# Kernel tuning notes

Hardware: AMD Instinct MI355X
Metric: run time of the kernel (lower is better)

## Reference

```python
import jax, jax.numpy as jnp
import numpy as np

B, N, M, C, KV, H = 2, 1024, 2048, 1024, 768, 16
D = C // H
SCALE = D ** -0.5  # qk_scale defaults to head_dim**-0.5


def setup_inputs() -> dict:
    key = jax.random.key(0)
    ks = jax.random.split(key, 8)
    return {
        "q": jax.random.normal(ks[0], (B, N, C), jnp.float32),
        "kv": jax.random.normal(ks[1], (B, M, KV), jnp.float32),
        "alibi_bias": jax.random.normal(ks[2], (B, H, N, M), jnp.float32) * 0.02,
        "padding_mask": jax.random.randint(ks[3], (B, M), 0, 2).astype(bool),
        "Wq": jax.random.normal(ks[4], (C, C), jnp.float32) * 0.02,
        "Wkv": jax.random.normal(ks[5], (2 * C, KV), jnp.float32) * 0.02,
        "Wproj": jax.random.normal(ks[6], (C, C), jnp.float32) * 0.02,
        "bproj": jnp.zeros((C,), jnp.float32),
    }


def reference(q, kv, alibi_bias, Wq, Wkv, Wproj, bproj, padding_mask):
    Bq, Nq, Cq = q.shape
    # q projection -> (B, H, N, D)
    qh = (q @ Wq.T).reshape(Bq, Nq, H, D).transpose(0, 2, 1, 3)
    # kv projection -> (2, B, H, M, D)
    kvp = (kv @ Wkv.T).reshape(Bq, -1, 2, H, D).transpose(2, 0, 3, 1, 4)
    k, v = kvp[0], kvp[1]
    # scaled dot-product scores (B, H, N, M)
    attn = jnp.einsum('bhnd,bhmd->bhnm', qh * SCALE, k)
    attn = attn + alibi_bias
    attn = jnp.where(padding_mask[:, None, None, :], -jnp.inf, attn)
    # softmax in fp32, cast back to q dtype (matches torch softmax(dtype=float32))
    attn = jax.nn.softmax(attn.astype(jnp.float32), axis=-1).astype(q.dtype)
    x = jnp.einsum('bhnm,bhmd->bhnd', attn, v).transpose(0, 2, 1, 3).reshape(Bq, Nq, Cq)
    return x @ Wproj.T + bproj
```

## Files before the change

### kernel.cpp

```cpp
#include <hip/hip_runtime.h>
#include <hip/hip_bf16.h>
#include <hip/hip_fp16.h>

#define B_  2
#define N_  1024
#define M_  2048
#define C_  1024
#define KV_ 768
#define H_  16
#define D_  64

typedef _Float16 half8 __attribute__((ext_vector_type(8)));
typedef float f32x4 __attribute__((ext_vector_type(4)));

__device__ inline void gload16(const _Float16* g, _Float16* l) {
    __builtin_amdgcn_global_load_lds(
        (const __attribute__((address_space(1))) unsigned int*)g,
        (__attribute__((address_space(3))) unsigned int*)l, 16, 0, 0);
}

#define NQ4  (B_ * N_ * C_ / 4)
#define NKV4 (B_ * M_ * KV_ / 4)
#define NWQ4 (C_ * C_ / 4)
#define NWK4 (2 * C_ * KV_ / 4)
#define NTOT4 (NQ4 + NKV4 + NWQ4 + NWK4 + NWQ4)

__global__ __launch_bounds__(256)
void cvt_all(const float* __restrict__ q, const float* __restrict__ kv,
             const float* __restrict__ Wq, const float* __restrict__ Wkv,
             const float* __restrict__ Wp,
             _Float16* __restrict__ qh, _Float16* __restrict__ kvh,
             _Float16* __restrict__ Wqh, _Float16* __restrict__ Wkvh,
             _Float16* __restrict__ Wph)
{
    int i = blockIdx.x * 256 + threadIdx.x;
    if (i >= NTOT4) return;
    const float* s; _Float16* d; int off; float sc = 1.0f;
    if (i < NQ4)                          { s = q;   d = qh;   off = i; sc = 0.125f; }
    else if (i < NQ4 + NKV4)              { s = kv;  d = kvh;  off = i - NQ4; }
    else if (i < NQ4 + NKV4 + NWQ4)       { s = Wq;  d = Wqh;  off = i - NQ4 - NKV4; }
    else if (i < NQ4 + NKV4 + NWQ4 + NWK4){ s = Wkv; d = Wkvh; off = i - NQ4 - NKV4 - NWQ4; }
    else                                  { s = Wp;  d = Wph;  off = i - NQ4 - NKV4 - NWQ4 - NWK4; }
    float4 v = ((const float4*)s)[off];
    union { _Float16 h[4]; unsigned long long u; } pk;
    pk.h[0] = (_Float16)(v.x * sc); pk.h[1] = (_Float16)(v.y * sc);
    pk.h[2] = (_Float16)(v.z * sc); pk.h[3] = (_Float16)(v.w * sc);
    ((unsigned long long*)d)[off] = pk.u;
}

template<int ND, int KD, int EPI>
__device__ __forceinline__
void gemm_body(const _Float16* A, const _Float16* Bm, void* out0, void* out1,
               _Float16* As, _Float16* Bs, int bx, int by)
{
    const int tid  = threadIdx.x;
    const int lane = tid & 63;
    const int w    = tid >> 6;
    const int l16  = lane & 15;
    const int quad = lane >> 4;
    const int wm   = w >> 1, wn = w & 1;
    const int m0   = by * 128;
    const int n0   = bx * 128;

    const int srow = tid >> 2;
    const int scol = ((tid & 3) ^ (srow & 3)) * 8;
    const int ldso = srow * 32 + (tid & 3) * 8;

    f32x4 acc[4][4];
    {
        f32x4 z = {0.f, 0.f, 0.f, 0.f};
        for (int i = 0; i < 4; i++) for (int j = 0; j < 4; j++) acc[i][j] = z;
    }

    for (int k0 = 0; k0 < KD; k0 += 32) {
        __syncthreads();
        gload16(A  + (size_t)(m0 + srow)      * KD + k0 + scol, As + ldso);
        gload16(A  + (size_t)(m0 + 64 + srow) * KD + k0 + scol, As + 64 * 32 + ldso);
        gload16(Bm + (size_t)(n0 + srow)      * KD + k0 + scol, Bs + ldso);
        gload16(Bm + (size_t)(n0 + 64 + srow) * KD + k0 + scol, Bs + 64 * 32 + ldso);
        __syncthreads();

        half8 af[4], bf[4];
        #pragma unroll
        for (int i = 0; i < 4; i++) {
            int r = wm * 64 + i * 16 + l16;
            af[i] = *(const half8*)&As[r * 32 + ((quad ^ (r & 3)) * 8)];
        }
        #pragma unroll
        for (int j = 0; j < 4; j++) {
            int r = wn * 64 + j * 16 + l16;
            bf[j] = *(const half8*)&Bs[r * 32 + ((quad ^ (r & 3)) * 8)];
        }
        #pragma unroll
        for (int i = 0; i < 4; i++)
            #pragma unroll
            for (int j = 0; j < 4; j++)
                acc[i][j] = __builtin_amdgcn_mfma_f32_16x16x32_f16(af[i], bf[j], acc[i][j], 0, 0, 0);
    }

    #pragma unroll
    for (int i = 0; i < 4; i++)
        #pragma unroll
        for (int j = 0; j < 4; j++) {
            int mb = m0 + wm * 64 + i * 16 + quad * 4;
            int n  = n0 + wn * 64 + j * 16 + l16;
            if (EPI == 0) {
                #pragma unroll
                for (int r = 0; r < 4; r++)
                    ((_Float16*)out0)[(size_t)(mb + r) * ND + n] = (_Float16)acc[i][j][r];
            } else {
                int b = mb >> 11, ml = mb & 2047;
                if (n < C_) {
                    int h = n >> 6, d = n & 63;
                    #pragma unroll
                    for (int r = 0; r < 4; r++)
                        ((_Float16*)out0)[((size_t)(b * H_ + h) * M_ + ml + r) * D_ + d] =
                            (_Float16)acc[i][j][r];
                } else {
                    int h = (n >> 6) & 15, d = n & 63;
                    union { _Float16 h4[4]; unsigned long long u; } pk;
                    #pragma unroll
                    for (int r = 0; r < 4; r++) pk.h4[r] = (_Float16)acc[i][j][r];
                    *(unsigned long long*)&((_Float16*)out1)[((size_t)(b * H_ + h) * D_ + d) * M_ + ml] = pk.u;
                }
            }
        }
}

__global__ __launch_bounds__(256)
void qkv_gemm(const _Float16* __restrict__ qh, const _Float16* __restrict__ Wqh,
              _Float16* __restrict__ qp,
              const _Float16* __restrict__ kvh, const _Float16* __restrict__ Wkvh,
              _Float16* __restrict__ k_ws, _Float16* __restrict__ v_ws)
{
    __shared__ _Float16 As[128 * 32];
    __shared__ _Float16 Bs[128 * 32];
    int id = blockIdx.x;
    if (id < 128)
        gemm_body<C_, C_, 0>(qh, Wqh, qp, nullptr, As, Bs, id & 7, id >> 3);
    else {
        int r = id - 128;
        gemm_body<2 * C_, KV_, 1>(kvh, Wkvh, k_ws, v_ws, As, Bs, r & 15, r >> 4);
    }
}

__global__ __launch_bounds__(256)
void outproj(const _Float16* __restrict__ A, const _Float16* __restrict__ Bm,
             float* __restrict__ out, const float* __restrict__ bias)
{
    __shared__ _Float16 As[64 * 32];
    __shared__ _Float16 Bs[64 * 32];

    const int tid  = threadIdx.x;
    const int lane = tid & 63;
    const int w    = tid >> 6;
    const int l16  = lane & 15;
    const int quad = lane >> 4;
    const int wm   = w >> 1, wn = w & 1;
    const int m0   = blockIdx.y * 64;
    const int n0   = blockIdx.x * 64;

    const int srow = tid >> 2;
    const int scol = ((tid & 3) ^ (srow & 3)) * 8;
    const int ldso = srow * 32 + (tid & 3) * 8;

    f32x4 acc[2][2];
    {
        f32x4 z = {0.f, 0.f, 0.f, 0.f};
        for (int i = 0; i < 2; i++) for (int j = 0; j < 2; j++) acc[i][j] = z;
    }

    for (int k0 = 0; k0 < C_; k0 += 32) {
        __syncthreads();
        gload16(A  + (size_t)(m0 + srow) * C_ + k0 + scol, As + ldso);
        gload16(Bm + (size_t)(n0 + srow) * C_ + k0 + scol, Bs + ldso);
        __syncthreads();

        half8 af[2], bf[2];
        #pragma unroll
        for (int i = 0; i < 2; i++) {
            int r = wm * 32 + i * 16 + l16;
            af[i] = *(const half8*)&As[r * 32 + ((quad ^ (r & 3)) * 8)];
        }
        #pragma unroll
        for (int j = 0; j < 2; j++) {
            int r = wn * 32 + j * 16 + l16;
            bf[j] = *(const half8*)&Bs[r * 32 + ((quad ^ (r & 3)) * 8)];
        }
        #pragma unroll
        for (int i = 0; i < 2; i++)
            #pragma unroll
            for (int j = 0; j < 2; j++)
                acc[i][j] = __builtin_amdgcn_mfma_f32_16x16x32_f16(af[i], bf[j], acc[i][j], 0, 0, 0);
    }

    #pragma unroll
    for (int i = 0; i < 2; i++)
        #pragma unroll
        for (int j = 0; j < 2; j++)
            #pragma unroll
            for (int r = 0; r < 4; r++) {
                int m = m0 + wm * 32 + i * 16 + quad * 4 + r;
                int n = n0 + wn * 32 + j * 16 + l16;
                out[(size_t)m * C_ + n] = acc[i][j][r] + bias[n];
            }
}

__global__ __launch_bounds__(256)
void flash_attn(const _Float16* __restrict__ qw, const _Float16* __restrict__ kw,
                const _Float16* __restrict__ vw, const float* __restrict__ alibi,
                const void* __restrict__ pmask, _Float16* __restrict__ xw)
{
    __shared__ _Float16 Ks[128 * 64];
    __shared__ _Float16 Vs[64 * 128];
    __shared__ _Float16 Ps[4][16][136];
    __shared__ int mflag;

    const int tid  = threadIdx.x;
    const int lane = tid & 63;
    const int w    = tid >> 6;
    const int l16  = lane & 15;
    const int quad = lane >> 4;
    const int bh   = blockIdx.y;
    const int b    = bh >> 4;
    const int h    = bh & 15;
    const int n0   = blockIdx.x * 64;

    if (tid < 64) {
        unsigned a = ((const unsigned*)pmask)[tid] & 0xFFFFFF00u;
        unsigned long long anyset = __ballot(a != 0);
        if (tid == 0) mflag = (anyset == 0ull) ? 1 : 0;
    }
    __syncthreads();
    const int mi = mflag;

    half8 qf[2];
    {
        const _Float16* qp = qw + ((size_t)(b * N_ + n0 + w * 16 + l16) * C_) + h * 64 + quad * 8;
        qf[0] = *(const half8*)qp;
        qf[1] = *(const half8*)(qp + 32);
    }

    f32x4 accO[4];
    float rs[4];
    {
        f32x4 z = {0.f, 0.f, 0.f, 0.f};
        for (int i = 0; i < 4; i++) accO[i] = z;
    }
    #pragma unroll
    for (int r = 0; r < 4; r++) rs[r] = 0.f;

    const _Float16* kbase = kw + (size_t)bh * (M_ * D_);
    const _Float16* vbase = vw + (size_t)bh * (D_ * M_);
    const float*    abase = alibi + (size_t)bh * ((size_t)N_ * M_) + (size_t)n0 * M_
                          + (size_t)(w * 16 + quad * 4) * M_;
    const unsigned char* pm8  = (const unsigned char*)pmask;
    const int*           pm32 = (const int*)pmask;

    for (int m0 = 0; m0 < M_; m0 += 128) {
        __syncthreads();
        #pragma unroll
        for (int i = 0; i < 4; i++) {
            int idx = tid + 256 * i;
            int kr = idx >> 3, kp = idx & 7;
            gload16(kbase + (size_t)(m0 + kr) * D_ + ((kp ^ (kr & 7)) * 8), Ks + idx * 8);
            int vr = idx >> 4, vp = idx & 15;
            gload16(vbase + (size_t)vr * M_ + m0 + ((vp ^ (vr & 15)) * 8), Vs + idx * 8);
        }
        __syncthreads();

        float al[8][4];
        int   mk[8];
        #pragma unroll
        for (int j = 0; j < 8; j++) {
            int mcol = m0 + j * 16 + l16;
            mk[j] = mi ? pm32[b * M_ + mcol] : (int)pm8[b * M_ + mcol];
            const float* ap = abase + mcol;
            #pragma unroll
            for (int r = 0; r < 4; r++) al[j][r] = ap[(size_t)r * M_];
        }

        f32x4 s[8];
        {
            f32x4 z = {0.f, 0.f, 0.f, 0.f};
            for (int j = 0; j < 8; j++) s[j] = z;
        }
        #pragma unroll
        for (int j = 0; j < 8; j++) {
            int row = j * 16 + l16;
            half8 kf0 = *(const half8*)&Ks[row * 64 + ((quad ^ (row & 7)) * 8)];
            half8 kf1 = *(const half8*)&Ks[row * 64 + (((4 + quad) ^ (row & 7)) * 8)];
            s[j] = __builtin_amdgcn_mfma_f32_16x16x32_f16(qf[0], kf0, s[j], 0, 0, 0);
            s[j] = __builtin_amdgcn_mfma_f32_16x16x32_f16(qf[1], kf1, s[j], 0, 0, 0);
        }

        #pragma unroll
        for (int j = 0; j < 8; j++)
            #pragma unroll
            for (int r = 0; r < 4; r++) {
                float sv = fminf(s[j][r] + al[j][r], 11.0f);
                float p  = exp2f(sv * 1.44269504f);
                p = mk[j] ? 0.f : p;
                rs[r] += p;
                Ps[w][quad * 4 + r][j * 16 + l16] = (_Float16)p;
            }

        #pragma unroll
        for (int kk = 0; kk < 4; kk++) {
            half8 pf = *(const half8*)&Ps[w][l16][kk * 32 + quad * 8];
            #pragma unroll
            for (int dt = 0; dt < 4; dt++) {
                int vrow = dt * 16 + l16;
                half8 vf = *(const half8*)&Vs[vrow * 128 + (((kk * 4 + quad) ^ (vrow & 15)) * 8)];
                accO[dt] = __builtin_amdgcn_mfma_f32_16x16x32_f16(pf, vf, accO[dt], 0, 0, 0);
            }
        }
    }

    #pragma unroll
    for (int off = 1; off < 16; off <<= 1)
        #pragma unroll
        for (int r = 0; r < 4; r++) rs[r] += __shfl_xor(rs[r], off, 64);
    float inv[4];
    #pragma unroll
    for (int r = 0; r < 4; r++) inv[r] = 1.0f / rs[r];

    #pragma unroll
    for (int dt = 0; dt < 4; dt++)
        #pragma unroll
        for (int r = 0; r < 4; r++) {
            int n = n0 + w * 16 + quad * 4 + r;
            xw[(size_t)(b * N_ + n) * C_ + h * 64 + dt * 16 + l16] =
                (_Float16)(accO[dt][r] * inv[r]);
        }
}

extern "C" void kernel_launch(void* const* d_in, const int* in_sizes, int n_in,
                              void* d_out, int out_size, void* d_ws, size_t ws_size,
                              hipStream_t stream)
{
    const float* q     = (const float*)d_in[0];
    const float* kv    = (const float*)d_in[1];
    const float* alibi = (const float*)d_in[2];
    const void*  pmask = d_in[3];
    const float* Wq    = (const float*)d_in[4];
    const float* Wkv   = (const float*)d_in[5];
    const float* Wproj = (const float*)d_in[6];
    const float* bproj = (const float*)d_in[7];
    float* out = (float*)d_out;

    const size_t MB = 1u << 20;
    char* ws = (char*)d_ws;
    _Float16* qh     = (_Float16*)(ws + 0 * MB);
    _Float16* kvh    = (_Float16*)(ws + 4 * MB);
    _Float16* Wqh    = (_Float16*)(ws + 12 * MB);
    _Float16* Wkvh   = (_Float16*)(ws + 14 * MB);
    _Float16* Wprojh = (_Float16*)(ws + 18 * MB);
    _Float16* qp     = (_Float16*)(ws + 20 * MB);
    _Float16* k_ws   = (_Float16*)(ws + 24 * MB);
    _Float16* v_ws   = (_Float16*)(ws + 33 * MB);
    _Float16* x_ws   = (_Float16*)(ws + 42 * MB);

    cvt_all<<<(NTOT4 + 255) / 256, 256, 0, stream>>>(
        q, kv, Wq, Wkv, Wproj, qh, kvh, Wqh, Wkvh, Wprojh);

    qkv_gemm<<<640, 256, 0, stream>>>(qh, Wqh, qp, kvh, Wkvh, k_ws, v_ws);

    flash_attn<<<dim3(N_ / 64, B_ * H_), 256, 0, stream>>>(
        qp, k_ws, v_ws, alibi, pmask, x_ws);

    outproj<<<dim3(C_ / 64, (B_ * N_) / 64), 256, 0, stream>>>(
        x_ws, Wprojh, out, bproj);
}
```

Before: 461.6 us.

## Fuse all stages into one persistent kernel with software grid barriers

Replaces the four separate launches (convert, QKV GEMM, flash attention, output projection) with a single persistent kernel of 512 blocks that runs each stage in turn, separated by atomic-counter grid barriers. The QKV GEMM tiles are spread over the fixed grid, with the first 128 blocks taking a second tile. The aim is to remove inter-kernel launch gaps and drain/fill bubbles. In exchange it relies on all 512 blocks being co-resident (launch bounds of 2 blocks per CU), adds a zeroing launch and spin-wait barriers with a timeout break, and may limit registers for the attention stage.

```diff
diff --git a/kernel.cpp b/kernel.cpp
--- a/kernel.cpp
+++ b/kernel.cpp
@@ -10,6 +10,8 @@
 #define H_  16
 #define D_  64
 
+#define NBLK 512
+
 typedef _Float16 half8 __attribute__((ext_vector_type(8)));
 typedef float f32x4 __attribute__((ext_vector_type(4)));
 
@@ -25,27 +27,25 @@
 #define NWK4 (2 * C_ * KV_ / 4)
 #define NTOT4 (NQ4 + NKV4 + NWQ4 + NWK4 + NWQ4)
 
-__global__ __launch_bounds__(256)
-void cvt_all(const float* __restrict__ q, const float* __restrict__ kv,
-             const float* __restrict__ Wq, const float* __restrict__ Wkv,
-             const float* __restrict__ Wp,
-             _Float16* __restrict__ qh, _Float16* __restrict__ kvh,
-             _Float16* __restrict__ Wqh, _Float16* __restrict__ Wkvh,
-             _Float16* __restrict__ Wph)
-{
-    int i = blockIdx.x * 256 + threadIdx.x;
-    if (i >= NTOT4) return;
-    const float* s; _Float16* d; int off; float sc = 1.0f;
-    if (i < NQ4)                          { s = q;   d = qh;   off = i; sc = 0.125f; }
-    else if (i < NQ4 + NKV4)              { s = kv;  d = kvh;  off = i - NQ4; }
-    else if (i < NQ4 + NKV4 + NWQ4)       { s = Wq;  d = Wqh;  off = i - NQ4 - NKV4; }
-    else if (i < NQ4 + NKV4 + NWQ4 + NWK4){ s = Wkv; d = Wkvh; off = i - NQ4 - NKV4 - NWQ4; }
-    else                                  { s = Wp;  d = Wph;  off = i - NQ4 - NKV4 - NWQ4 - NWK4; }
-    float4 v = ((const float4*)s)[off];
-    union { _Float16 h[4]; unsigned long long u; } pk;
-    pk.h[0] = (_Float16)(v.x * sc); pk.h[1] = (_Float16)(v.y * sc);
-    pk.h[2] = (_Float16)(v.z * sc); pk.h[3] = (_Float16)(v.w * sc);
-    ((unsigned long long*)d)[off] = pk.u;
+__device__ __forceinline__ void grid_barrier(unsigned int* bar, unsigned int target)
+{
+    __syncthreads();
+    if (threadIdx.x == 0) {
+        __threadfence();
+        __hip_atomic_fetch_add(bar, 1u, __ATOMIC_RELEASE, __HIP_MEMORY_SCOPE_AGENT);
+        int spins = 0;
+        while (__hip_atomic_load(bar, __ATOMIC_ACQUIRE, __HIP_MEMORY_SCOPE_AGENT) < target) {
+            __builtin_amdgcn_s_sleep(16);
+            if (++spins > 100000) break;
+        }
+    }
+    __syncthreads();
+    __threadfence();
+}
+
+__global__ void zero_bar(unsigned int* bar)
+{
+    if (threadIdx.x == 0) *bar = 0;
 }
 
 template<int ND, int KD, int EPI>
@@ -127,212 +127,240 @@
         }
 }
 
-__global__ __launch_bounds__(256)
-void qkv_gemm(const _Float16* __restrict__ qh, const _Float16* __restrict__ Wqh,
-              _Float16* __restrict__ qp,
-              const _Float16* __restrict__ kvh, const _Float16* __restrict__ Wkvh,
-              _Float16* __restrict__ k_ws, _Float16* __restrict__ v_ws)
-{
-    __shared__ _Float16 As[128 * 32];
-    __shared__ _Float16 Bs[128 * 32];
-    int id = blockIdx.x;
-    if (id < 128)
-        gemm_body<C_, C_, 0>(qh, Wqh, qp, nullptr, As, Bs, id & 7, id >> 3);
-    else {
-        int r = id - 128;
-        gemm_body<2 * C_, KV_, 1>(kvh, Wkvh, k_ws, v_ws, As, Bs, r & 15, r >> 4);
-    }
-}
-
-__global__ __launch_bounds__(256)
-void outproj(const _Float16* __restrict__ A, const _Float16* __restrict__ Bm,
-             float* __restrict__ out, const float* __restrict__ bias)
-{
-    __shared__ _Float16 As[64 * 32];
-    __shared__ _Float16 Bs[64 * 32];
-
-    const int tid  = threadIdx.x;
-    const int lane = tid & 63;
-    const int w    = tid >> 6;
-    const int l16  = lane & 15;
-    const int quad = lane >> 4;
-    const int wm   = w >> 1, wn = w & 1;
-    const int m0   = blockIdx.y * 64;
-    const int n0   = blockIdx.x * 64;
-
-    const int srow = tid >> 2;
-    const int scol = ((tid & 3) ^ (srow & 3)) * 8;
-    const int ldso = srow * 32 + (tid & 3) * 8;
-
-    f32x4 acc[2][2];
+#define SMEM_BYTES 50192
+
+__global__ __launch_bounds__(256, 2)
+void fused(const float* __restrict__ q, const float* __restrict__ kv,
+           const float* __restrict__ alibi, const void* __restrict__ pmask,
+           const float* __restrict__ Wq, const float* __restrict__ Wkv,
+           const float* __restrict__ Wp, const float* __restrict__ bias,
+           float* __restrict__ out,
+           _Float16* __restrict__ qh, _Float16* __restrict__ kvh,
+           _Float16* __restrict__ Wqh, _Float16* __restrict__ Wkvh,
+           _Float16* __restrict__ Wph,
+           _Float16* __restrict__ qp, _Float16* __restrict__ k_ws,
+           _Float16* __restrict__ v_ws, _Float16* __restrict__ x_ws,
+           unsigned int* __restrict__ bar)
+{
+    __shared__ __align__(16) unsigned char smem[SMEM_BYTES];
+    const int tid = threadIdx.x;
+    const int bid = blockIdx.x;
+
+    for (int i = bid * 256 + tid; i < NTOT4; i += NBLK * 256) {
+        const float* s; _Float16* d; int off; float sc = 1.0f;
+        if (i < NQ4)                          { s = q;   d = qh;   off = i; sc = 0.125f; }
+        else if (i < NQ4 + NKV4)              { s = kv;  d = kvh;  off = i - NQ4; }
+        else if (i < NQ4 + NKV4 + NWQ4)       { s = Wq;  d = Wqh;  off = i - NQ4 - NKV4; }
+        else if (i < NQ4 + NKV4 + NWQ4 + NWK4){ s = Wkv; d = Wkvh; off = i - NQ4 - NKV4 - NWQ4; }
+        else                                  { s = Wp;  d = Wph;  off = i - NQ4 - NKV4 - NWQ4 - NWK4; }
+        float4 v = ((const float4*)s)[off];
+        union { _Float16 h[4]; unsigned long long u; } pk;
+        pk.h[0] = (_Float16)(v.x * sc); pk.h[1] = (_Float16)(v.y * sc);
+        pk.h[2] = (_Float16)(v.z * sc); pk.h[3] = (_Float16)(v.w * sc);
+        ((unsigned long long*)d)[off] = pk.u;
+    }
+    grid_barrier(bar, NBLK);
+
     {
-        f32x4 z = {0.f, 0.f, 0.f, 0.f};
-        for (int i = 0; i < 2; i++) for (int j = 0; j < 2; j++) acc[i][j] = z;
-    }
-
-    for (int k0 = 0; k0 < C_; k0 += 32) {
+        _Float16* As = (_Float16*)smem;
+        _Float16* Bs = (_Float16*)(smem + 128 * 32 * 2);
+        int t = (bid < 384) ? (128 + bid) : (bid - 384);
+        for (;;) {
+            if (t < 128)
+                gemm_body<C_, C_, 0>(qh, Wqh, qp, nullptr, As, Bs, t & 7, t >> 3);
+            else {
+                int r = t - 128;
+                gemm_body<2 * C_, KV_, 1>(kvh, Wkvh, k_ws, v_ws, As, Bs, r & 15, r >> 4);
+            }
+            if (bid < 128 && t < 512) { t = 512 + bid; continue; }
+            break;
+        }
+    }
+    grid_barrier(bar, 2 * NBLK);
+
+    {
+        _Float16* Ks = (_Float16*)(smem);
+        _Float16* Vs = (_Float16*)(smem + 16384);
+        _Float16* Ps = (_Float16*)(smem + 32768);
+        int* mflagp  = (int*)(smem + 50176);
+
+        const int lane = tid & 63;
+        const int w    = tid >> 6;
+        const int l16  = lane & 15;
+        const int quad = lane >> 4;
+        const int wk = (bid & 7) * 64 + (bid >> 3);
+        const int bh = wk >> 4;
+        const int b  = bh >> 4;
+        const int h  = bh & 15;
+        const int n0 = (wk & 15) * 64;
+
+        if (tid < 64) {
+            unsigned a = ((const unsigned*)pmask)[tid] & 0xFFFFFF00u;
+            unsigned long long anyset = __ballot(a != 0);
+            if (tid == 0) *mflagp = (anyset == 0ull) ? 1 : 0;
+        }
         __syncthreads();
-        gload16(A  + (size_t)(m0 + srow) * C_ + k0 + scol, As + ldso);
-        gload16(Bm + (size_t)(n0 + srow) * C_ + k0 + scol, Bs + ldso);
-        __syncthreads();
-
-        half8 af[2], bf[2];
-        #pragma unroll
-        for (int i = 0; i < 2; i++) {
-            int r = wm * 32 + i * 16 + l16;
-            af[i] = *(const half8*)&As[r * 32 + ((quad ^ (r & 3)) * 8)];
-        }
-        #pragma unroll
-        for (int j = 0; j < 2; j++) {
-            int r = wn * 32 + j * 16 + l16;
-            bf[j] = *(const half8*)&Bs[r * 32 + ((quad ^ (r & 3)) * 8)];
-        }
-        #pragma unroll
-        for (int i = 0; i < 2; i++)
-            #pragma unroll
-            for (int j = 0; j < 2; j++)
-                acc[i][j] = __builtin_amdgcn_mfma_f32_16x16x32_f16(af[i], bf[j], acc[i][j], 0, 0, 0);
-    }
-
-    #pragma unroll
-    for (int i = 0; i < 2; i++)
-        #pragma unroll
-        for (int j = 0; j < 2; j++)
-            #pragma unroll
-            for (int r = 0; r < 4; r++) {
-                int m = m0 + wm * 32 + i * 16 + quad * 4 + r;
-                int n = n0 + wn * 32 + j * 16 + l16;
-                out[(size_t)m * C_ + n] = acc[i][j][r] + bias[n];
-            }
-}
-
-__global__ __launch_bounds__(256)
-void flash_attn(const _Float16* __restrict__ qw, const _Float16* __restrict__ kw,
-                const _Float16* __restrict__ vw, const float* __restrict__ alibi,
-                const void* __restrict__ pmask, _Float16* __restrict__ xw)
-{
-    __shared__ _Float16 Ks[128 * 64];
-    __shared__ _Float16 Vs[64 * 128];
-    __shared__ _Float16 Ps[4][16][136];
-    __shared__ int mflag;
-
-    const int tid  = threadIdx.x;
-    const int lane = tid & 63;
-    const int w    = tid >> 6;
-    const int l16  = lane & 15;
-    const int quad = lane >> 4;
-    const int bh   = blockIdx.y;
-    const int b    = bh >> 4;
-    const int h    = bh & 15;
-    const int n0   = blockIdx.x * 64;
-
-    if (tid < 64) {
-        unsigned a = ((const unsigned*)pmask)[tid] & 0xFFFFFF00u;
-        unsigned long long anyset = __ballot(a != 0);
-        if (tid == 0) mflag = (anyset == 0ull) ? 1 : 0;
-    }
-    __syncthreads();
-    const int mi = mflag;
-
-    half8 qf[2];
-    {
-        const _Float16* qp = qw + ((size_t)(b * N_ + n0 + w * 16 + l16) * C_) + h * 64 + quad * 8;
-        qf[0] = *(const half8*)qp;
-        qf[1] = *(const half8*)(qp + 32);
-    }
-
-    f32x4 accO[4];
-    float rs[4];
-    {
-        f32x4 z = {0.f, 0.f, 0.f, 0.f};
-        for (int i = 0; i < 4; i++) accO[i] = z;
-    }
-    #pragma unroll
-    for (int r = 0; r < 4; r++) rs[r] = 0.f;
-
-    const _Float16* kbase = kw + (size_t)bh * (M_ * D_);
-    const _Float16* vbase = vw + (size_t)bh * (D_ * M_);
-    const float*    abase = alibi + (size_t)bh * ((size_t)N_ * M_) + (size_t)n0 * M_
-                          + (size_t)(w * 16 + quad * 4) * M_;
-    const unsigned char* pm8  = (const unsigned char*)pmask;
-    const int*           pm32 = (const int*)pmask;
-
-    for (int m0 = 0; m0 < M_; m0 += 128) {
-        __syncthreads();
-        #pragma unroll
-        for (int i = 0; i < 4; i++) {
-            int idx = tid + 256 * i;
-            int kr = idx >> 3, kp = idx & 7;
-            gload16(kbase + (size_t)(m0 + kr) * D_ + ((kp ^ (kr & 7)) * 8), Ks + idx * 8);
-            int vr = idx >> 4, vp = idx & 15;
-            gload16(vbase + (size_t)vr * M_ + m0 + ((vp ^ (vr & 15)) * 8), Vs + idx * 8);
-        }
-        __syncthreads();
-
-        float al[8][4];
-        int   mk[8];
-        #pragma unroll
-        for (int j = 0; j < 8; j++) {
-            int mcol = m0 + j * 16 + l16;
-            mk[j] = mi ? pm32[b * M_ + mcol] : (int)pm8[b * M_ + mcol];
-            const float* ap = abase + mcol;
-            #pragma unroll
-            for (int r = 0; r < 4; r++) al[j][r] = ap[(size_t)r * M_];
-        }
-
-        f32x4 s[8];
+        const int mi = *mflagp;
+
+        half8 qf[2];
+        {
+            const _Float16* qptr = qp + ((size_t)(b * N_ + n0 + w * 16 + l16) * C_) + h * 64 + quad * 8;
+            qf[0] = *(const half8*)qptr;
+            qf[1] = *(const half8*)(qptr + 32);
+        }
+
+        f32x4 accO[4];
+        float rs[4];
         {
             f32x4 z = {0.f, 0.f, 0.f, 0.f};
-            for (int j = 0; j < 8; j++) s[j] = z;
-        }
-        #pragma unroll
-        for (int j = 0; j < 8; j++) {
-            int row = j * 16 + l16;
-            half8 kf0 = *(const half8*)&Ks[row * 64 + ((quad ^ (row & 7)) * 8)];
-            half8 kf1 = *(const half8*)&Ks[row * 64 + (((4 + quad) ^ (row & 7)) * 8)];
-            s[j] = __builtin_amdgcn_mfma_f32_16x16x32_f16(qf[0], kf0, s[j], 0, 0, 0);
-            s[j] = __builtin_amdgcn_mfma_f32_16x16x32_f16(qf[1], kf1, s[j], 0, 0, 0);
-        }
-
-        #pragma unroll
-        for (int j = 0; j < 8; j++)
+            for (int i = 0; i < 4; i++) accO[i] = z;
+        }
+        #pragma unroll
+        for (int r = 0; r < 4; r++) rs[r] = 0.f;
+
+        const _Float16* kbase = k_ws + (size_t)bh * (M_ * D_);
+        const _Float16* vbase = v_ws + (size_t)bh * (D_ * M_);
+        const float*    abase = alibi + (size_t)bh * ((size_t)N_ * M_) + (size_t)n0 * M_
+                              + (size_t)(w * 16 + quad * 4) * M_;
+        const unsigned char* pm8  = (const unsigned char*)pmask;
+        const int*           pm32 = (const int*)pmask;
+
+        for (int m0 = 0; m0 < M_; m0 += 128) {
+            __syncthreads();
+            #pragma unroll
+            for (int i = 0; i < 4; i++) {
+                int idx = tid + 256 * i;
+                int kr = idx >> 3, kp = idx & 7;
+                gload16(kbase + (size_t)(m0 + kr) * D_ + ((kp ^ (kr & 7)) * 8), Ks + idx * 8);
+                int vr = idx >> 4, vp = idx & 15;
+                gload16(vbase + (size_t)vr * M_ + m0 + ((vp ^ (vr & 15)) * 8), Vs + idx * 8);
+            }
+            __syncthreads();
+
+            float al[8][4];
+            int   mk[8];
+            #pragma unroll
+            for (int j = 0; j < 8; j++) {
+                int mcol = m0 + j * 16 + l16;
+                mk[j] = mi ? pm32[b * M_ + mcol] : (int)pm8[b * M_ + mcol];
+                const float* ap = abase + mcol;
+                #pragma unroll
+                for (int r = 0; r < 4; r++) al[j][r] = ap[(size_t)r * M_];
+            }
+
+            f32x4 s[8];
+            {
+                f32x4 z = {0.f, 0.f, 0.f, 0.f};
+                for (int j = 0; j < 8; j++) s[j] = z;
+            }
+            #pragma unroll
+            for (int j = 0; j < 8; j++) {
+                int row = j * 16 + l16;
+                half8 kf0 = *(const half8*)&Ks[row * 64 + ((quad ^ (row & 7)) * 8)];
+                half8 kf1 = *(const half8*)&Ks[row * 64 + (((4 + quad) ^ (row & 7)) * 8)];
+                s[j] = __builtin_amdgcn_mfma_f32_16x16x32_f16(qf[0], kf0, s[j], 0, 0, 0);
+                s[j] = __builtin_amdgcn_mfma_f32_16x16x32_f16(qf[1], kf1, s[j], 0, 0, 0);
+            }
+
+            #pragma unroll
+            for (int j = 0; j < 8; j++)
+                #pragma unroll
+                for (int r = 0; r < 4; r++) {
+                    float sv = fminf(s[j][r] + al[j][r], 11.0f);
+                    float p  = exp2f(sv * 1.44269504f);
+                    p = mk[j] ? 0.f : p;
+                    rs[r] += p;
+                    Ps[(w * 16 + quad * 4 + r) * 136 + j * 16 + l16] = (_Float16)p;
+                }
+
+            #pragma unroll
+            for (int kk = 0; kk < 4; kk++) {
+                half8 pf = *(const half8*)&Ps[(w * 16 + l16) * 136 + kk * 32 + quad * 8];
+                #pragma unroll
+                for (int dt = 0; dt < 4; dt++) {
+                    int vrow = dt * 16 + l16;
+                    half8 vf = *(const half8*)&Vs[vrow * 128 + (((kk * 4 + quad) ^ (vrow & 15)) * 8)];
+                    accO[dt] = __builtin_amdgcn_mfma_f32_16x16x32_f16(pf, vf, accO[dt], 0, 0, 0);
+                }
+            }
+        }
+
+        #pragma unroll
+        for (int off = 1; off < 16; off <<= 1)
+            #pragma unroll
+            for (int r = 0; r < 4; r++) rs[r] += __shfl_xor(rs[r], off, 64);
+        float inv[4];
+        #pragma unroll
+        for (int r = 0; r < 4; r++) inv[r] = 1.0f / rs[r];
+
+        #pragma unroll
+        for (int dt = 0; dt < 4; dt++)
             #pragma unroll
             for (int r = 0; r < 4; r++) {
-                float sv = fminf(s[j][r] + al[j][r], 11.0f);
-                float p  = exp2f(sv * 1.44269504f);
-                p = mk[j] ? 0.f : p;
-                rs[r] += p;
-                Ps[w][quad * 4 + r][j * 16 + l16] = (_Float16)p;
-            }
-
-        #pragma unroll
-        for (int kk = 0; kk < 4; kk++) {
-            half8 pf = *(const half8*)&Ps[w][l16][kk * 32 + quad * 8];
-            #pragma unroll
-            for (int dt = 0; dt < 4; dt++) {
-                int vrow = dt * 16 + l16;
-                half8 vf = *(const half8*)&Vs[vrow * 128 + (((kk * 4 + quad) ^ (vrow & 15)) * 8)];
-                accO[dt] = __builtin_amdgcn_mfma_f32_16x16x32_f16(pf, vf, accO[dt], 0, 0, 0);
-            }
-        }
-    }
-
-    #pragma unroll
-    for (int off = 1; off < 16; off <<= 1)
-        #pragma unroll
-        for (int r = 0; r < 4; r++) rs[r] += __shfl_xor(rs[r], off, 64);
-    float inv[4];
-    #pragma unroll
-    for (int r = 0; r < 4; r++) inv[r] = 1.0f / rs[r];
-
-    #pragma unroll
-    for (int dt = 0; dt < 4; dt++)
-        #pragma unroll
-        for (int r = 0; r < 4; r++) {
-            int n = n0 + w * 16 + quad * 4 + r;
-            xw[(size_t)(b * N_ + n) * C_ + h * 64 + dt * 16 + l16] =
-                (_Float16)(accO[dt][r] * inv[r]);
-        }
+                int n = n0 + w * 16 + quad * 4 + r;
+                x_ws[(size_t)(b * N_ + n) * C_ + h * 64 + dt * 16 + l16] =
+                    (_Float16)(accO[dt][r] * inv[r]);
+            }
+    }
+    grid_barrier(bar, 3 * NBLK);
+
+    {
+        _Float16* As = (_Float16*)smem;
+        _Float16* Bs = (_Float16*)(smem + 64 * 32 * 2);
+
+        const int lane = tid & 63;
+        const int w    = tid >> 6;
+        const int l16  = lane & 15;
+        const int quad = lane >> 4;
+        const int wm   = w >> 1, wn = w & 1;
+        const int m0   = (bid >> 4) * 64;
+        const int n0   = (bid & 15) * 64;
+
+        const int srow = tid >> 2;
+        const int scol = ((tid & 3) ^ (srow & 3)) * 8;
+        const int ldso = srow * 32 + (tid & 3) * 8;
+
+        f32x4 acc[2][2];
+        {
+            f32x4 z = {0.f, 0.f, 0.f, 0.f};
+            for (int i = 0; i < 2; i++) for (int j = 0; j < 2; j++) acc[i][j] = z;
+        }
+
+        for (int k0 = 0; k0 < C_; k0 += 32) {
+            __syncthreads();
+            gload16(x_ws + (size_t)(m0 + srow) * C_ + k0 + scol, As + ldso);
+            gload16(Wph  + (size_t)(n0 + srow) * C_ + k0 + scol, Bs + ldso);
+            __syncthreads();
+
+            half8 af[2], bf[2];
+            #pragma unroll
+            for (int i = 0; i < 2; i++) {
+                int r = wm * 32 + i * 16 + l16;
+                af[i] = *(const half8*)&As[r * 32 + ((quad ^ (r & 3)) * 8)];
+            }
+            #pragma unroll
+            for (int j = 0; j < 2; j++) {
+                int r = wn * 32 + j * 16 + l16;
+                bf[j] = *(const half8*)&Bs[r * 32 + ((quad ^ (r & 3)) * 8)];
+            }
+            #pragma unroll
+            for (int i = 0; i < 2; i++)
+                #pragma unroll
+                for (int j = 0; j < 2; j++)
+                    acc[i][j] = __builtin_amdgcn_mfma_f32_16x16x32_f16(af[i], bf[j], acc[i][j], 0, 0, 0);
+        }
+
+        #pragma unroll
+        for (int i = 0; i < 2; i++)
+            #pragma unroll
+            for (int j = 0; j < 2; j++)
+                #pragma unroll
+                for (int r = 0; r < 4; r++) {
+                    int m = m0 + wm * 32 + i * 16 + quad * 4 + r;
+                    int n = n0 + wn * 32 + j * 16 + l16;
+                    out[(size_t)m * C_ + n] = acc[i][j][r] + bias[n];
+                }
+    }
 }
 
 extern "C" void kernel_launch(void* const* d_in, const int* in_sizes, int n_in,
@@ -360,15 +388,10 @@
     _Float16* k_ws   = (_Float16*)(ws + 24 * MB);
     _Float16* v_ws   = (_Float16*)(ws + 33 * MB);
     _Float16* x_ws   = (_Float16*)(ws + 42 * MB);
-
-    cvt_all<<<(NTOT4 + 255) / 256, 256, 0, stream>>>(
-        q, kv, Wq, Wkv, Wproj, qh, kvh, Wqh, Wkvh, Wprojh);
-
-    qkv_gemm<<<640, 256, 0, stream>>>(qh, Wqh, qp, kvh, Wkvh, k_ws, v_ws);
-
-    flash_attn<<<dim3(N_ / 64, B_ * H_), 256, 0, stream>>>(
-        qp, k_ws, v_ws, alibi, pmask, x_ws);
-
-    outproj<<<dim3(C_ / 64, (B_ * N_) / 64), 256, 0, stream>>>(
-        x_ws, Wprojh, out, bproj);
-}
+    unsigned int* bar = (unsigned int*)(ws + 63 * MB);
+
+    zero_bar<<<1, 64, 0, stream>>>(bar);
+    fused<<<NBLK, 256, 0, stream>>>(
+        q, kv, alibi, pmask, Wq, Wkv, Wproj, bproj, out,
+        qh, kvh, Wqh, Wkvh, Wprojh, qp, k_ws, v_ws, x_ws, bar);
+}
```

Result: slower. 824.5 us (+78.6%).

## Read K/V directly from global in attention, remap blocks across XCDs, stream alibi nontemporally

Applied to the files above, without the earlier changes.

The attention kernel no longer stages K and V tiles in shared memory with barriers. Each wave now loads its MFMA operands straight from global memory and relies on L2 for reuse. The grid becomes 1D with a block-index swizzle so that blocks sharing a (batch, head) land on the same XCD's L2, and the alibi bias is read with nontemporal loads to avoid polluting the cache. This removes the LDS traffic and both per-iteration __syncthreads. In exchange, each of the four waves refetches the same K/V data from cache, and the global loads are less coalesced.

```diff
diff --git a/kernel.cpp b/kernel.cpp
--- a/kernel.cpp
+++ b/kernel.cpp
@@ -211,28 +211,23 @@
                 const _Float16* __restrict__ vw, const float* __restrict__ alibi,
                 const void* __restrict__ pmask, _Float16* __restrict__ xw)
 {
-    __shared__ _Float16 Ks[128 * 64];
-    __shared__ _Float16 Vs[64 * 128];
     __shared__ _Float16 Ps[4][16][136];
-    __shared__ int mflag;
 
     const int tid  = threadIdx.x;
     const int lane = tid & 63;
     const int w    = tid >> 6;
     const int l16  = lane & 15;
     const int quad = lane >> 4;
-    const int bh   = blockIdx.y;
-    const int b    = bh >> 4;
-    const int h    = bh & 15;
-    const int n0   = blockIdx.x * 64;
-
-    if (tid < 64) {
-        unsigned a = ((const unsigned*)pmask)[tid] & 0xFFFFFF00u;
-        unsigned long long anyset = __ballot(a != 0);
-        if (tid == 0) mflag = (anyset == 0ull) ? 1 : 0;
-    }
-    __syncthreads();
-    const int mi = mflag;
+
+    const int bid = blockIdx.x;
+    const int wk  = (bid & 7) * 64 + (bid >> 3);
+    const int bh  = wk >> 4;
+    const int b   = bh >> 4;
+    const int h   = bh & 15;
+    const int n0  = (wk & 15) * 64;
+
+    unsigned am = ((const unsigned*)pmask)[lane] & 0xFFFFFF00u;
+    const int mi = (__ballot(am != 0) == 0ull) ? 1 : 0;
 
     half8 qf[2];
     {
@@ -258,17 +253,6 @@
     const int*           pm32 = (const int*)pmask;
 
     for (int m0 = 0; m0 < M_; m0 += 128) {
-        __syncthreads();
-        #pragma unroll
-        for (int i = 0; i < 4; i++) {
-            int idx = tid + 256 * i;
-            int kr = idx >> 3, kp = idx & 7;
-            gload16(kbase + (size_t)(m0 + kr) * D_ + ((kp ^ (kr & 7)) * 8), Ks + idx * 8);
-            int vr = idx >> 4, vp = idx & 15;
-            gload16(vbase + (size_t)vr * M_ + m0 + ((vp ^ (vr & 15)) * 8), Vs + idx * 8);
-        }
-        __syncthreads();
-
         float al[8][4];
         int   mk[8];
         #pragma unroll
@@ -277,7 +261,8 @@
             mk[j] = mi ? pm32[b * M_ + mcol] : (int)pm8[b * M_ + mcol];
             const float* ap = abase + mcol;
             #pragma unroll
-            for (int r = 0; r < 4; r++) al[j][r] = ap[(size_t)r * M_];
+            for (int r = 0; r < 4; r++)
+                al[j][r] = __builtin_nontemporal_load(ap + (size_t)r * M_);
         }
 
         f32x4 s[8];
@@ -288,8 +273,9 @@
         #pragma unroll
         for (int j = 0; j < 8; j++) {
             int row = j * 16 + l16;
-            half8 kf0 = *(const half8*)&Ks[row * 64 + ((quad ^ (row & 7)) * 8)];
-            half8 kf1 = *(const half8*)&Ks[row * 64 + (((4 + quad) ^ (row & 7)) * 8)];
+            const _Float16* kp = kbase + (size_t)(m0 + row) * D_ + quad * 8;
+            half8 kf0 = *(const half8*)kp;
+            half8 kf1 = *(const half8*)(kp + 32);
             s[j] = __builtin_amdgcn_mfma_f32_16x16x32_f16(qf[0], kf0, s[j], 0, 0, 0);
             s[j] = __builtin_amdgcn_mfma_f32_16x16x32_f16(qf[1], kf1, s[j], 0, 0, 0);
         }
@@ -310,8 +296,8 @@
             half8 pf = *(const half8*)&Ps[w][l16][kk * 32 + quad * 8];
             #pragma unroll
             for (int dt = 0; dt < 4; dt++) {
-                int vrow = dt * 16 + l16;
-                half8 vf = *(const half8*)&Vs[vrow * 128 + (((kk * 4 + quad) ^ (vrow & 15)) * 8)];
+                const _Float16* vp = vbase + (size_t)(dt * 16 + l16) * M_ + m0 + kk * 32 + quad * 8;
+                half8 vf = *(const half8*)vp;
                 accO[dt] = __builtin_amdgcn_mfma_f32_16x16x32_f16(pf, vf, accO[dt], 0, 0, 0);
             }
         }
@@ -366,7 +352,7 @@
 
     qkv_gemm<<<640, 256, 0, stream>>>(qh, Wqh, qp, kvh, Wkvh, k_ws, v_ws);
 
-    flash_attn<<<dim3(N_ / 64, B_ * H_), 256, 0, stream>>>(
+    flash_attn<<<512, 256, 0, stream>>>(
         qp, k_ws, v_ws, alibi, pmask, x_ws);
 
     outproj<<<dim3(C_ / 64, (B_ * N_) / 64), 256, 0, stream>>>(
```

Result: slower. 531.7 us (+15.2%).
